# Kernel optimization log

Measured on AMD Instinct MI355X. Metric: run time of the kernel, lower is better.

## Reference

```python
import jax, jax.numpy as jnp
import numpy as np

INPUT_DIM = 1024
HIDDEN_DIM = 2048
NUM_EMB = 4096
EMB_DIM = 256
N = 65536


def setup_inputs() -> dict:
    key = jax.random.key(0)
    ks = jax.random.split(key, 10)
    s = lambda fan_in: 1.0 / np.sqrt(fan_in)
    return {
        "x": jax.random.normal(ks[0], (N, INPUT_DIM), dtype=jnp.float32),
        # encoder: Linear(input_dim, hidden) -> ReLU -> Linear(hidden, emb)
        "W1": jax.random.uniform(ks[1], (INPUT_DIM, HIDDEN_DIM), jnp.float32, -s(INPUT_DIM), s(INPUT_DIM)),
        "b1": jax.random.uniform(ks[2], (HIDDEN_DIM,), jnp.float32, -s(INPUT_DIM), s(INPUT_DIM)),
        "W2": jax.random.uniform(ks[3], (HIDDEN_DIM, EMB_DIM), jnp.float32, -s(HIDDEN_DIM), s(HIDDEN_DIM)),
        "b2": jax.random.uniform(ks[4], (EMB_DIM,), jnp.float32, -s(HIDDEN_DIM), s(HIDDEN_DIM)),
        # codebook (nn.Embedding weight)
        "codebook": jax.random.normal(ks[5], (NUM_EMB, EMB_DIM), dtype=jnp.float32),
        # decoder: Linear(emb, hidden) -> ReLU -> Linear(hidden, input_dim)
        "W3": jax.random.uniform(ks[6], (EMB_DIM, HIDDEN_DIM), jnp.float32, -s(EMB_DIM), s(EMB_DIM)),
        "b3": jax.random.uniform(ks[7], (HIDDEN_DIM,), jnp.float32, -s(EMB_DIM), s(EMB_DIM)),
        "W4": jax.random.uniform(ks[8], (HIDDEN_DIM, INPUT_DIM), jnp.float32, -s(HIDDEN_DIM), s(HIDDEN_DIM)),
        "b4": jax.random.uniform(ks[9], (INPUT_DIM,), jnp.float32, -s(HIDDEN_DIM), s(HIDDEN_DIM)),
    }


def reference(x, W1, b1, W2, b2, codebook, W3, b3, W4, b4):
    # encoder
    h = jax.nn.relu(x @ W1 + b1)
    encoded = h @ W2 + b2                      # [N, E]
    # cdist (squared form; argmin is identical to Euclidean argmin)
    enc_sq = jnp.sum(encoded * encoded, axis=-1, keepdims=True)   # [N, 1]
    cb_sq = jnp.sum(codebook * codebook, axis=-1)                 # [K]
    d2 = enc_sq - 2.0 * (encoded @ codebook.T) + cb_sq            # [N, K]
    indices = jnp.argmin(d2, axis=-1)                             # [N]
    quantized = codebook[indices]                                 # [N, E]
    # decoder
    h2 = jax.nn.relu(quantized @ W3 + b3)
    decoded = h2 @ W4 + b4
    return (quantized, decoded)
```

## Files before the change

### kernel.cpp

```cpp
#include <hip/hip_runtime.h>

#define N_ROWS 65536
#define IN_DIM 1024
#define HID    2048
#define EMB    256
#define NCODE  4096

typedef __attribute__((ext_vector_type(8))) short bf16x8;
typedef __attribute__((ext_vector_type(4))) float f32x4;

__device__ __forceinline__ unsigned short f2bf(float v) {
    unsigned u = __float_as_uint(v);
    u += 0x7FFFu + ((u >> 16) & 1u);
    return (unsigned short)(u >> 16);
}
__device__ __forceinline__ float bf2f(unsigned short h) {
    return __uint_as_float(((unsigned)h) << 16);
}
__device__ __forceinline__ void gload16(const unsigned short* g, unsigned short* l) {
    __builtin_amdgcn_global_load_lds(
        (const __attribute__((address_space(1))) unsigned int*)g,
        (__attribute__((address_space(3))) unsigned int*)l, 16, 0, 0);
}

template<int SPLIT>
__global__ __launch_bounds__(256) void k_conv_w(
    const float* __restrict__ src, unsigned short* __restrict__ dh,
    unsigned short* __restrict__ dl, int NC, int nkt)
{
    const int t = threadIdx.x;
    const int nt = blockIdx.x, kt = blockIdx.y;
    const int kk = t >> 2, j4 = (t & 3) << 2;
    const int k0 = kt << 6, n0 = nt << 4;
    float4 v = *(const float4*)(src + (size_t)(k0 + kk) * NC + n0 + j4);
    size_t tb = ((size_t)nt * nkt + kt) * 1024 + ((kk >> 3) * 128) + (kk & 7);
    float vv[4] = {v.x, v.y, v.z, v.w};
    #pragma unroll
    for (int j = 0; j < 4; ++j) {
        unsigned short h = f2bf(vv[j]);
        dh[tb + (size_t)(j4 + j) * 8] = h;
        if (SPLIT) dl[tb + (size_t)(j4 + j) * 8] = f2bf(vv[j] - bf2f(h));
    }
}

__global__ __launch_bounds__(256) void k_conv_a(
    const float* __restrict__ src, unsigned short* __restrict__ dst, int Kw, int nkt)
{
    const int t = threadIdx.x;
    const int mt = blockIdx.x, kt = blockIdx.y;
    const int rr = t >> 4, k4 = (t & 15) << 2;
    float4 v = *(const float4*)(src + (size_t)(mt * 16 + rr) * Kw + kt * 64 + k4);
    size_t addr = ((size_t)mt * nkt + kt) * 1024 + (k4 >> 3) * 128 + rr * 8 + (k4 & 7);
    ushort4 h = { f2bf(v.x), f2bf(v.y), f2bf(v.z), f2bf(v.w) };
    *(ushort4*)&dst[addr] = h;
}

__global__ __launch_bounds__(256) void k_conv_cb(
    const float* __restrict__ cb, unsigned short* __restrict__ ch,
    unsigned short* __restrict__ cl_, float* __restrict__ halfsq)
{
    const int t = threadIdx.x;
    const int ct = blockIdx.x;
    const int cl = t >> 4, f = t & 15;
    const int code = (ct << 4) + cl;
    float ssq = 0.f;
    #pragma unroll
    for (int it = 0; it < 4; ++it) {
        const int k4 = (f << 2) + (it << 6);
        float4 v = *(const float4*)(cb + (size_t)code * EMB + k4);
        ssq += v.x * v.x + v.y * v.y + v.z * v.z + v.w * v.w;
        size_t tb = ((size_t)(ct * 4 + (k4 >> 6))) * 1024 + ((k4 >> 3) & 7) * 128 + cl * 8 + (k4 & 7);
        ushort4 h = { f2bf(v.x), f2bf(v.y), f2bf(v.z), f2bf(v.w) };
        *(ushort4*)&ch[tb] = h;
        ushort4 lo = { f2bf(v.x - bf2f(h.x)), f2bf(v.y - bf2f(h.y)),
                       f2bf(v.z - bf2f(h.z)), f2bf(v.w - bf2f(h.w)) };
        *(ushort4*)&cl_[tb] = lo;
    }
    #pragma unroll
    for (int off = 1; off <= 8; off <<= 1) ssq += __shfl_xor(ssq, off);
    if (f == 0) halfsq[code] = 0.5f * ssq;
}

template<int SPLIT, int AFMT, int OUTT>
__global__ __launch_bounds__(512, 1) void k_layer2(
    const float* __restrict__ A, const unsigned short* __restrict__ At,
    const unsigned short* __restrict__ Atl, int a_nkt,
    int lda, int K,
    const unsigned short* __restrict__ Bh, const unsigned short* __restrict__ Bl,
    int b_nkt, const float* __restrict__ bias, int biasoff,
    float* __restrict__ out, unsigned short* __restrict__ outt,
    unsigned short* __restrict__ outt2,
    int outw, int relu, int init, int ny_log2)
{
    constexpr int BUFSZ = SPLIT ? 32768 : 24576;
    constexpr int AL = 8192;
    constexpr int BH = SPLIT ? 16384 : 8192;
    __shared__ __align__(16) unsigned short s_mem[2 * BUFSZ];

    const int t = threadIdx.x;
    const int id = blockIdx.x;
    const int m_low = id & 7, rest = id >> 3;
    const int nb = rest & ((1 << ny_log2) - 1);
    const int m0 = (((rest >> ny_log2) << 3) | m_low) * 128;
    const int nb0 = nb * 256;
    const int lane = t & 63, wv = t >> 6;
    const int wm = wv >> 2, wn = wv & 3;
    const int g = lane >> 4, rr = lane & 15;
    const int nt = K >> 6;

    f32x4 acc[4][4];
    #pragma unroll
    for (int mi = 0; mi < 4; ++mi)
        #pragma unroll
        for (int ni = 0; ni < 4; ++ni) acc[mi][ni] = (f32x4){0.f, 0.f, 0.f, 0.f};

    #define STAGE_DMA(buf, ktile)                                                      \
        {                                                                              \
            unsigned short* base_ = &s_mem[(buf) * BUFSZ];                             \
            _Pragma("unroll")                                                          \
            for (int jj = 0; jj < 2; ++jj) {                                           \
                const int j_ = wv * 2 + jj;                                            \
                const size_t gt_ = ((size_t)(nb0 / 16 + j_) * b_nkt + (ktile)) * 1024; \
                _Pragma("unroll")                                                      \
                for (int hf = 0; hf < 2; ++hf)                                         \
                    gload16(Bh + gt_ + hf * 512 + lane * 8,                            \
                            base_ + BH + j_ * 1024 + hf * 512);                        \
            }                                                                          \
            if (AFMT >= 1) {                                                           \
                const size_t ga_ = ((size_t)(m0 / 16 + wv) * a_nkt + (ktile)) * 1024;  \
                _Pragma("unroll")                                                      \
                for (int hf = 0; hf < 2; ++hf)                                         \
                    gload16(At + ga_ + hf * 512 + lane * 8,                            \
                            base_ + wv * 1024 + hf * 512);                             \
                if (AFMT == 2) {                                                       \
                    _Pragma("unroll")                                                  \
                    for (int hf = 0; hf < 2; ++hf)                                     \
                        gload16(Atl + ga_ + hf * 512 + lane * 8,                       \
                                base_ + AL + wv * 1024 + hf * 512);                    \
                }                                                                      \
            }                                                                          \
        }

    #define A_LOAD(ktile, pv)                                                          \
        {                                                                              \
            _Pragma("unroll")                                                          \
            for (int it = 0; it < 4; ++it) {                                           \
                int f_ = t + (it << 9);                                                \
                int r_ = f_ >> 4, k4_ = (f_ & 15) << 2;                                \
                pv[it] = *(const float4*)(A + (size_t)(m0 + r_) * lda + (ktile) * 64 + k4_); \
            }                                                                          \
        }

    #define A_WRITE(buf, pv)                                                           \
        {                                                                              \
            unsigned short* base_ = &s_mem[(buf) * BUFSZ];                             \
            _Pragma("unroll")                                                          \
            for (int it = 0; it < 4; ++it) {                                           \
                int f_ = t + (it << 9);                                                \
                int r_ = f_ >> 4, k4_ = (f_ & 15) << 2;                                \
                int mt_ = r_ >> 4, rl_ = r_ & 15, kb_ = k4_ >> 3, e_ = k4_ & 7;        \
                int addr_ = mt_ * 1024 + kb_ * 128 + ((rl_ ^ kb_) << 3) + e_;          \
                float4 v_ = pv[it];                                                    \
                ushort4 hi_, lo_;                                                      \
                hi_.x = f2bf(v_.x); hi_.y = f2bf(v_.y); hi_.z = f2bf(v_.z); hi_.w = f2bf(v_.w); \
                *(ushort4*)&base_[addr_] = hi_;                                        \
                if (SPLIT) {                                                           \
                    lo_.x = f2bf(v_.x - bf2f(hi_.x)); lo_.y = f2bf(v_.y - bf2f(hi_.y)); \
                    lo_.z = f2bf(v_.z - bf2f(hi_.z)); lo_.w = f2bf(v_.w - bf2f(hi_.w)); \
                    *(ushort4*)&base_[AL + addr_] = lo_;                               \
                }                                                                      \
            }                                                                          \
        }

    #define COMPUTE(buf, ktile)                                                        \
        {                                                                              \
            const unsigned short* base_ = &s_mem[(buf) * BUFSZ];                       \
            __builtin_amdgcn_s_setprio(1);                                             \
            _Pragma("unroll")                                                          \
            for (int s = 0; s < 2; ++s) {                                              \
                const int kb = (s << 2) + g;                                           \
                bf16x8 a_h[4], a_l[4], b_h[4], b_l[4];                                 \
                _Pragma("unroll")                                                      \
                for (int i = 0; i < 4; ++i) {                                          \
                    int arow = (AFMT == 0) ? (((rr ^ kb) & 15) << 3) : (rr << 3);      \
                    int aaddr = (wm * 4 + i) * 1024 + kb * 128 + arow;                 \
                    a_h[i] = *(const bf16x8*)&base_[aaddr];                            \
                    if (SPLIT) a_l[i] = *(const bf16x8*)&base_[AL + aaddr];            \
                    int baddr = (wn * 4 + i) * 1024 + kb * 128 + (rr << 3);            \
                    b_h[i] = *(const bf16x8*)&base_[BH + baddr];                       \
                    if (SPLIT)                                                         \
                        b_l[i] = *(const bf16x8*)(Bl +                                 \
                            ((size_t)(nb0 / 16 + wn * 4 + i) * b_nkt + (ktile)) * 1024 \
                            + kb * 128 + (rr << 3));                                   \
                }                                                                      \
                _Pragma("unroll")                                                      \
                for (int mi = 0; mi < 4; ++mi)                                         \
                    _Pragma("unroll")                                                  \
                    for (int ni = 0; ni < 4; ++ni) {                                   \
                        acc[mi][ni] = __builtin_amdgcn_mfma_f32_16x16x32_bf16(a_h[mi], b_h[ni], acc[mi][ni], 0, 0, 0); \
                        if (SPLIT) {                                                   \
                            acc[mi][ni] = __builtin_amdgcn_mfma_f32_16x16x32_bf16(a_l[mi], b_h[ni], acc[mi][ni], 0, 0, 0); \
                            acc[mi][ni] = __builtin_amdgcn_mfma_f32_16x16x32_bf16(a_h[mi], b_l[ni], acc[mi][ni], 0, 0, 0); \
                        }                                                              \
                    }                                                                  \
            }                                                                          \
            __builtin_amdgcn_s_setprio(0);                                             \
        }

    float4 pv[4];
    STAGE_DMA(0, 0)
    if (AFMT == 0) {
        A_LOAD(0, pv)
        A_WRITE(0, pv)
    }
    asm volatile("s_waitcnt vmcnt(0) lgkmcnt(0)" ::: "memory");
    __builtin_amdgcn_s_barrier();
    __builtin_amdgcn_sched_barrier(0);

    int cur = 0;
    for (int kt = 0; kt < nt; ++kt) {
        if (kt + 1 < nt) {
            STAGE_DMA(cur ^ 1, kt + 1)
            if (AFMT == 0) A_LOAD(kt + 1, pv)
        }
        COMPUTE(cur, kt)
        if (AFMT == 0) { if (kt + 1 < nt) A_WRITE(cur ^ 1, pv) }
        asm volatile("s_waitcnt vmcnt(0) lgkmcnt(0)" ::: "memory");
        __builtin_amdgcn_s_barrier();
        __builtin_amdgcn_sched_barrier(0);
        cur ^= 1;
    }
    #undef STAGE_DMA
    #undef A_LOAD
    #undef A_WRITE
    #undef COMPUTE

    if (OUTT == 0) {
        float* sf = (float*)s_mem;
        for (int rm = 0; rm < 2; ++rm) {
            if (wm == rm) {
                #pragma unroll
                for (int mi = 0; mi < 4; ++mi)
                    #pragma unroll
                    for (int ni = 0; ni < 4; ++ni)
                        #pragma unroll
                        for (int rg = 0; rg < 4; ++rg)
                            sf[(mi * 16 + g * 4 + rg) * 256 + wn * 64 + ni * 16 + rr] = acc[mi][ni][rg];
            }
            __syncthreads();
            #pragma unroll
            for (int it = 0; it < 8; ++it) {
                int f = t + (it << 9);
                int r = f >> 6, c4 = (f & 63) << 2;
                float4 v = *(const float4*)&sf[r * 256 + c4];
                int gr = m0 + rm * 64 + r, gc = nb0 + c4;
                float* op = out + (size_t)gr * outw + gc;
                if (init) {
                    v.x += bias[biasoff + gc + 0]; v.y += bias[biasoff + gc + 1];
                    v.z += bias[biasoff + gc + 2]; v.w += bias[biasoff + gc + 3];
                } else {
                    float4 o = *(const float4*)op;
                    v.x += o.x; v.y += o.y; v.z += o.z; v.w += o.w;
                }
                if (relu) {
                    v.x = fmaxf(v.x, 0.f); v.y = fmaxf(v.y, 0.f);
                    v.z = fmaxf(v.z, 0.f); v.w = fmaxf(v.w, 0.f);
                }
                *(float4*)op = v;
            }
            __syncthreads();
        }
    } else {
        const int npass = (OUTT == 2) ? 2 : 1;
        for (int pass = 0; pass < npass; ++pass) {
            #pragma unroll
            for (int mi = 0; mi < 4; ++mi)
                #pragma unroll
                for (int ni = 0; ni < 4; ++ni) {
                    const int c = wn * 64 + ni * 16 + rr;
                    float bb = bias[biasoff + nb0 + c];
                    #pragma unroll
                    for (int rg = 0; rg < 4; ++rg) {
                        float v = acc[mi][ni][rg] + bb;
                        if (relu) v = fmaxf(v, 0.f);
                        unsigned short hi = f2bf(v);
                        unsigned short w = (pass == 0) ? hi : f2bf(v - bf2f(hi));
                        int addr = ((wm * 4 + mi) * 4 + wn) * 1024
                                 + (ni * 2 + (rr >> 3)) * 128 + (g * 4 + rg) * 8 + (rr & 7);
                        s_mem[addr] = w;
                    }
                }
            __syncthreads();
            unsigned short* dst = (pass == 0) ? outt : outt2;
            #pragma unroll
            for (int it = 0; it < 8; ++it) {
                int f = t + (it << 9);
                int tl = f >> 7, w8 = f & 127;
                size_t gaddr = ((size_t)(m0 / 16 + (tl >> 2)) * outw + nb0 / 64 + (tl & 3)) * 1024;
                *(float4*)(dst + gaddr + w8 * 8) = *(const float4*)&s_mem[tl * 1024 + w8 * 8];
            }
            __syncthreads();
        }
    }
}

__global__ __launch_bounds__(512, 2) void k_dist(
    float* encq, const unsigned short* __restrict__ ch,
    const unsigned short* __restrict__ cl,
    const float* __restrict__ hsq, const float* __restrict__ cb)
{
    __shared__ __align__(16) unsigned short s_cb[2][16384];
    __shared__ int s_c1[256], s_c2[256];

    const int t = threadIdx.x;
    const int lane = t & 63, wv = t >> 6;
    const int g = lane >> 4, rr = lane & 15;
    const int r0 = blockIdx.x * 256;

    bf16x8 eh[2][8], el[2][8];
    #pragma unroll
    for (int rg = 0; rg < 2; ++rg) {
        const float* ep = encq + (size_t)(r0 + wv * 32 + rg * 16 + rr) * EMB + g * 8;
        #pragma unroll
        for (int s = 0; s < 8; ++s) {
            float4 v0 = *(const float4*)(ep + s * 32);
            float4 v1 = *(const float4*)(ep + s * 32 + 4);
            float vv[8] = {v0.x, v0.y, v0.z, v0.w, v1.x, v1.y, v1.z, v1.w};
            bf16x8 a, b;
            #pragma unroll
            for (int j = 0; j < 8; ++j) {
                unsigned short h = f2bf(vv[j]);
                a[j] = (short)h;
                b[j] = (short)f2bf(vv[j] - bf2f(h));
            }
            eh[rg][s] = a; el[rg][s] = b;
        }
    }
    float b1v[2][4], b2v[2][4]; int i1v[2][4], i2v[2][4];
    #pragma unroll
    for (int rg = 0; rg < 2; ++rg)
        #pragma unroll
        for (int r2 = 0; r2 < 4; ++r2) {
            b1v[rg][r2] = -1e30f; b2v[rg][r2] = -1e30f;
            i1v[rg][r2] = 0; i2v[rg][r2] = 0;
        }

    #define STAGE(buf, c)                                                              \
        {                                                                              \
            const unsigned short* gh_ = ch + (size_t)(c) * 8192 + wv * 1024;           \
            const unsigned short* gl_ = cl + (size_t)(c) * 8192 + wv * 1024;           \
            _Pragma("unroll")                                                          \
            for (int i_ = 0; i_ < 2; ++i_) {                                           \
                gload16(gh_ + i_ * 512 + lane * 8, &s_cb[buf][wv * 1024 + i_ * 512]);  \
                gload16(gl_ + i_ * 512 + lane * 8, &s_cb[buf][8192 + wv * 1024 + i_ * 512]); \
            }                                                                          \
        }

    #define COMPUTE(cur, c, hv_)                                                       \
        {                                                                              \
            f32x4 ahh[2][2], ahl[2][2], alh[2][2];                                     \
            _Pragma("unroll")                                                          \
            for (int rg = 0; rg < 2; ++rg)                                             \
                _Pragma("unroll")                                                      \
                for (int ci = 0; ci < 2; ++ci) {                                       \
                    ahh[rg][ci] = (f32x4){0.f, 0.f, 0.f, 0.f};                         \
                    ahl[rg][ci] = (f32x4){0.f, 0.f, 0.f, 0.f};                         \
                    alh[rg][ci] = (f32x4){0.f, 0.f, 0.f, 0.f};                         \
                }                                                                      \
            __builtin_amdgcn_s_setprio(1);                                             \
            _Pragma("unroll")                                                          \
            for (int s = 0; s < 8; ++s) {                                              \
                const int ktile = s >> 1, kb = ((s & 1) << 2) + g;                     \
                _Pragma("unroll")                                                      \
                for (int ci = 0; ci < 2; ++ci) {                                       \
                    const int off = (ci * 4 + ktile) * 1024 + kb * 128 + rr * 8;       \
                    bf16x8 bh = *(const bf16x8*)&s_cb[cur][off];                       \
                    bf16x8 bl = *(const bf16x8*)&s_cb[cur][8192 + off];                \
                    _Pragma("unroll")                                                  \
                    for (int rg = 0; rg < 2; ++rg) {                                   \
                        ahh[rg][ci] = __builtin_amdgcn_mfma_f32_16x16x32_bf16(eh[rg][s], bh, ahh[rg][ci], 0, 0, 0); \
                        ahl[rg][ci] = __builtin_amdgcn_mfma_f32_16x16x32_bf16(eh[rg][s], bl, ahl[rg][ci], 0, 0, 0); \
                        alh[rg][ci] = __builtin_amdgcn_mfma_f32_16x16x32_bf16(el[rg][s], bh, alh[rg][ci], 0, 0, 0); \
                    }                                                                  \
                }                                                                      \
            }                                                                          \
            __builtin_amdgcn_s_setprio(0);                                             \
            _Pragma("unroll")                                                          \
            for (int rg = 0; rg < 2; ++rg)                                             \
                _Pragma("unroll")                                                      \
                for (int ci = 0; ci < 2; ++ci) {                                       \
                    f32x4 av = ahh[rg][ci] + ahl[rg][ci] + alh[rg][ci];                \
                    const int code = ((c) << 5) + (ci << 4) + rr;                      \
                    const float hs = __shfl(hv_, ci * 16 + rr);                        \
                    _Pragma("unroll")                                                  \
                    for (int r2 = 0; r2 < 4; ++r2) {                                   \
                        float v = av[r2] - hs;                                         \
                        bool bt1 = (v > b1v[rg][r2]) || (v == b1v[rg][r2] && code < i1v[rg][r2]); \
                        bool bt2 = (v > b2v[rg][r2]) || (v == b2v[rg][r2] && code < i2v[rg][r2]); \
                        if (bt1) { b2v[rg][r2] = b1v[rg][r2]; i2v[rg][r2] = i1v[rg][r2]; \
                                   b1v[rg][r2] = v; i1v[rg][r2] = code; }              \
                        else if (bt2) { b2v[rg][r2] = v; i2v[rg][r2] = code; }         \
                    }                                                                  \
                }                                                                      \
        }

    STAGE(0, 0)
    int cur = 0;
    for (int c = 0; c < 127; ++c) {
        STAGE(cur ^ 1, c + 1)
        float hv_ = hsq[(c << 5) + (lane & 31)];
        asm volatile("s_waitcnt vmcnt(5)" ::: "memory");
        __builtin_amdgcn_s_barrier();
        __builtin_amdgcn_sched_barrier(0);
        COMPUTE(cur, c, hv_)
        asm volatile("" ::: "memory");
        __builtin_amdgcn_s_barrier();
        cur ^= 1;
    }
    {
        float hv_ = hsq[(127 << 5) + (lane & 31)];
        asm volatile("s_waitcnt vmcnt(0)" ::: "memory");
        __builtin_amdgcn_s_barrier();
        __builtin_amdgcn_sched_barrier(0);
        COMPUTE(cur, 127, hv_)
    }
    #undef STAGE
    #undef COMPUTE

    #pragma unroll
    for (int off = 1; off <= 8; off <<= 1) {
        #pragma unroll
        for (int rg = 0; rg < 2; ++rg)
            #pragma unroll
            for (int r2 = 0; r2 < 4; ++r2) {
                float ob1 = __shfl_xor(b1v[rg][r2], off), ob2 = __shfl_xor(b2v[rg][r2], off);
                int oi1 = __shfl_xor(i1v[rg][r2], off), oi2 = __shfl_xor(i2v[rg][r2], off);
                bool ofirst = (ob1 > b1v[rg][r2]) || (ob1 == b1v[rg][r2] && oi1 < i1v[rg][r2]);
                if (ofirst) {
                    bool mysec = (b1v[rg][r2] > ob2) || (b1v[rg][r2] == ob2 && i1v[rg][r2] < oi2);
                    b2v[rg][r2] = mysec ? b1v[rg][r2] : ob2; i2v[rg][r2] = mysec ? i1v[rg][r2] : oi2;
                    b1v[rg][r2] = ob1; i1v[rg][r2] = oi1;
                } else {
                    bool osec = (ob1 > b2v[rg][r2]) || (ob1 == b2v[rg][r2] && oi1 < i2v[rg][r2]);
                    b2v[rg][r2] = osec ? ob1 : b2v[rg][r2]; i2v[rg][r2] = osec ? oi1 : i2v[rg][r2];
                }
            }
    }
    if (rr == 0) {
        #pragma unroll
        for (int rg = 0; rg < 2; ++rg)
            #pragma unroll
            for (int r2 = 0; r2 < 4; ++r2) {
                int rl = wv * 32 + rg * 16 + g * 4 + r2;
                s_c1[rl] = i1v[rg][r2]; s_c2[rl] = i2v[rg][r2];
            }
    }
    __syncthreads();

    for (int rloc = 0; rloc < 32; ++rloc) {
        const int row = wv * 32 + rloc;
        const int c1 = s_c1[row], c2 = s_c2[row];
        float4 ev = *(const float4*)(encq + (size_t)(r0 + row) * EMB + lane * 4);
        float4 v1 = *(const float4*)(cb + (size_t)c1 * EMB + lane * 4);
        float4 v2 = *(const float4*)(cb + (size_t)c2 * EMB + lane * 4);
        float d1 = ev.x * v1.x + ev.y * v1.y + ev.z * v1.z + ev.w * v1.w;
        float d2 = ev.x * v2.x + ev.y * v2.y + ev.z * v2.z + ev.w * v2.w;
        #pragma unroll
        for (int off = 1; off <= 32; off <<= 1) {
            d1 += __shfl_xor(d1, off);
            d2 += __shfl_xor(d2, off);
        }
        if (lane == 0) {
            float s1 = d1 - hsq[c1], s2 = d2 - hsq[c2];
            bool keep1 = (s1 > s2) || (s1 == s2 && c1 < c2);
            s_c1[row] = keep1 ? c1 : c2;
        }
    }
    __syncthreads();
    #pragma unroll
    for (int it = 0; it < 32; ++it) {
        int f = t + (it << 9);
        int row = f >> 6, c4 = (f & 63) << 2;
        int bi = s_c1[row];
        *(float4*)(encq + (size_t)(r0 + row) * EMB + c4) =
            *(const float4*)(cb + (size_t)bi * EMB + c4);
    }
}

__global__ __launch_bounds__(256) void k_dec_fb(
    const float* __restrict__ qz,
    const float* __restrict__ W3, const float* __restrict__ b3,
    const float* __restrict__ W4, const float* __restrict__ b4,
    float* __restrict__ outd) {
    __shared__ float s_q[8][EMB];
    __shared__ float s_h2[8][HID];
    const int t = threadIdx.x;
    const int row0 = blockIdx.x * 8;
    #pragma unroll
    for (int r = 0; r < 8; ++r) s_q[r][t] = qz[(size_t)(row0 + r) * EMB + t];
    __syncthreads();
    for (int gg = 0; gg < 8; ++gg) {
        const int j = (gg << 8) + t;
        float acc[8];
        #pragma unroll
        for (int r = 0; r < 8; ++r) acc[r] = 0.f;
        const float* wp = W3 + j;
        for (int e = 0; e < EMB; e += 4) {
            const float w0 = wp[(size_t)(e + 0) * HID];
            const float w1v = wp[(size_t)(e + 1) * HID];
            const float w2v = wp[(size_t)(e + 2) * HID];
            const float w3v = wp[(size_t)(e + 3) * HID];
            #pragma unroll
            for (int r = 0; r < 8; ++r) {
                const float4 qv = *reinterpret_cast<const float4*>(&s_q[r][e]);
                acc[r] = fmaf(qv.x, w0, acc[r]);
                acc[r] = fmaf(qv.y, w1v, acc[r]);
                acc[r] = fmaf(qv.z, w2v, acc[r]);
                acc[r] = fmaf(qv.w, w3v, acc[r]);
            }
        }
        const float bb = b3[j];
        #pragma unroll
        for (int r = 0; r < 8; ++r) s_h2[r][j] = fmaxf(acc[r] + bb, 0.f);
    }
    __syncthreads();
    float acc4[8][4];
    #pragma unroll
    for (int r = 0; r < 8; ++r)
        #pragma unroll
        for (int ci = 0; ci < 4; ++ci) acc4[r][ci] = 0.f;
    const float* w4p = W4 + t;
    for (int k = 0; k < HID; k += 4) {
        float wv[4][4];
        #pragma unroll
        for (int ki = 0; ki < 4; ++ki)
            #pragma unroll
            for (int ci = 0; ci < 4; ++ci)
                wv[ki][ci] = w4p[(size_t)(k + ki) * IN_DIM + (ci << 8)];
        #pragma unroll
        for (int r = 0; r < 8; ++r) {
            const float4 hv = *reinterpret_cast<const float4*>(&s_h2[r][k]);
            #pragma unroll
            for (int ci = 0; ci < 4; ++ci) {
                acc4[r][ci] = fmaf(hv.x, wv[0][ci], acc4[r][ci]);
                acc4[r][ci] = fmaf(hv.y, wv[1][ci], acc4[r][ci]);
                acc4[r][ci] = fmaf(hv.z, wv[2][ci], acc4[r][ci]);
                acc4[r][ci] = fmaf(hv.w, wv[3][ci], acc4[r][ci]);
            }
        }
    }
    #pragma unroll
    for (int ci = 0; ci < 4; ++ci) {
        const float bb = b4[(ci << 8) + t];
        #pragma unroll
        for (int r = 0; r < 8; ++r)
            outd[(size_t)(row0 + r) * IN_DIM + (ci << 8) + t] = acc4[r][ci] + bb;
    }
}

extern "C" void kernel_launch(void* const* d_in, const int* in_sizes, int n_in,
                              void* d_out, int out_size, void* d_ws, size_t ws_size,
                              hipStream_t stream) {
    const float* x  = (const float*)d_in[0];
    const float* W1 = (const float*)d_in[1];
    const float* b1 = (const float*)d_in[2];
    const float* W2 = (const float*)d_in[3];
    const float* b2 = (const float*)d_in[4];
    const float* cb = (const float*)d_in[5];
    const float* W3 = (const float*)d_in[6];
    const float* b3 = (const float*)d_in[7];
    const float* W4 = (const float*)d_in[8];
    const float* b4 = (const float*)d_in[9];

    float* outq = (float*)d_out;
    float* outd = outq + (size_t)N_ROWS * EMB;

    unsigned short* ou = (unsigned short*)outd;
    unsigned short* W1Th = ou;
    unsigned short* W1Tl = ou + 2097152;
    unsigned short* W2Th = ou + 4194304;
    unsigned short* W2Tl = ou + 4718592;
    unsigned short* cbh  = ou + 5242880;
    unsigned short* cbl  = ou + 6291456;
    float* halfsq = outd + 3670016;
    unsigned short* h_hi = (unsigned short*)(outd + 4194304);
    unsigned short* h_lo = h_hi + 33554432;
    unsigned short* qt = (unsigned short*)(outd + 58720256);
    float* enc = outq;

    const bool fastdec = ws_size >= (size_t)72351744;
    unsigned short* W3Th = (unsigned short*)d_ws;
    unsigned short* W4Th = W3Th + 524288;
    unsigned short* h2t  = (unsigned short*)((char*)d_ws + 5242880);

    k_conv_w<1><<<dim3(128, 16), 256, 0, stream>>>(W1, W1Th, W1Tl, HID, 16);
    k_conv_w<1><<<dim3(16, 32), 256, 0, stream>>>(W2, W2Th, W2Tl, EMB, 32);
    k_conv_cb<<<256, 256, 0, stream>>>(cb, cbh, cbl, halfsq);
    if (fastdec) {
        k_conv_w<0><<<dim3(128, 4), 256, 0, stream>>>(W3, W3Th, nullptr, HID, 4);
        k_conv_w<0><<<dim3(64, 32), 256, 0, stream>>>(W4, W4Th, nullptr, IN_DIM, 32);
    }
    for (int q = 0; q < 4; ++q) {
        k_layer2<1, 0, 2><<<1024, 512, 0, stream>>>(
            x, nullptr, nullptr, 0, IN_DIM, IN_DIM,
            W1Th + (size_t)q * 524288, W1Tl + (size_t)q * 524288, 16,
            b1, q * 512, nullptr, h_hi, h_lo, 8, 1, 0, 1);
        k_layer2<1, 2, 0><<<512, 512, 0, stream>>>(
            nullptr, h_hi, h_lo, 8, 0, 512,
            W2Th + (size_t)q * 8192, W2Tl + (size_t)q * 8192, 32,
            b2, 0, enc, nullptr, nullptr, EMB, 0, q == 0, 0);
    }
    k_dist<<<256, 512, 0, stream>>>(enc, cbh, cbl, halfsq, cb);
    if (fastdec) {
        k_conv_a<<<dim3(4096, 4), 256, 0, stream>>>(outq, qt, EMB, 4);
        for (int s = 0; s < 4; ++s) {
            const size_t roff = (size_t)s * 16384;
            k_layer2<0, 1, 1><<<1024, 512, 0, stream>>>(
                nullptr, qt + (size_t)s * 4194304, nullptr, 4, 0, EMB,
                W3Th, nullptr, 4,
                b3, 0, nullptr, h2t, nullptr, 32, 1, 0, 3);
            k_layer2<0, 1, 0><<<512, 512, 0, stream>>>(
                nullptr, h2t, nullptr, 32, 0, HID,
                W4Th, nullptr, 32,
                b4, 0, outd + roff * IN_DIM, nullptr, nullptr, IN_DIM, 0, 1, 2);
        }
    } else {
        k_dec_fb<<<N_ROWS / 8, 256, 0, stream>>>(outq, W3, b3, W4, b4, outd);
    }
}
```

Baseline: 2.374 ms.

## Pre-convert x to split bf16 tiles and chunk encoder by row blocks

Adds a kernel that converts each quarter of x into pre-tiled hi/lo bf16 buffers. The encoder is then restructured from four hidden-dim column chunks into four row chunks, so each chunk computes the full hidden width and writes its slice of the embedding directly instead of accumulating partial sums across passes. This is meant to remove the repeated fp32 reads and conversion of x in every layer-1 pass and the read-modify-write accumulation into enc. In exchange it adds extra conversion launches and workspace traffic, and it only takes effect when the workspace is large enough.

```diff
diff --git a/kernel.cpp b/kernel.cpp
--- a/kernel.cpp
+++ b/kernel.cpp
@@ -53,6 +53,22 @@
     size_t addr = ((size_t)mt * nkt + kt) * 1024 + (k4 >> 3) * 128 + rr * 8 + (k4 & 7);
     ushort4 h = { f2bf(v.x), f2bf(v.y), f2bf(v.z), f2bf(v.w) };
     *(ushort4*)&dst[addr] = h;
+}
+
+__global__ __launch_bounds__(256) void k_conv_a2(
+    const float* __restrict__ src, unsigned short* __restrict__ dh,
+    unsigned short* __restrict__ dl, int Kw, int nkt)
+{
+    const int t = threadIdx.x;
+    const int mt = blockIdx.x, kt = blockIdx.y;
+    const int rr = t >> 4, k4 = (t & 15) << 2;
+    float4 v = *(const float4*)(src + (size_t)(mt * 16 + rr) * Kw + kt * 64 + k4);
+    size_t addr = ((size_t)mt * nkt + kt) * 1024 + (k4 >> 3) * 128 + rr * 8 + (k4 & 7);
+    ushort4 h = { f2bf(v.x), f2bf(v.y), f2bf(v.z), f2bf(v.w) };
+    ushort4 lo = { f2bf(v.x - bf2f(h.x)), f2bf(v.y - bf2f(h.y)),
+                   f2bf(v.z - bf2f(h.z)), f2bf(v.w - bf2f(h.w)) };
+    *(ushort4*)&dh[addr] = h;
+    *(ushort4*)&dl[addr] = lo;
 }
 
 __global__ __launch_bounds__(256) void k_conv_cb(
@@ -592,6 +608,8 @@
     unsigned short* W3Th = (unsigned short*)d_ws;
     unsigned short* W4Th = W3Th + 524288;
     unsigned short* h2t  = (unsigned short*)((char*)d_ws + 5242880);
+    unsigned short* xt_hi = h2t;
+    unsigned short* xt_lo = h2t + 16777216;
 
     k_conv_w<1><<<dim3(128, 16), 256, 0, stream>>>(W1, W1Th, W1Tl, HID, 16);
     k_conv_w<1><<<dim3(16, 32), 256, 0, stream>>>(W2, W2Th, W2Tl, EMB, 32);
@@ -600,15 +618,30 @@
         k_conv_w<0><<<dim3(128, 4), 256, 0, stream>>>(W3, W3Th, nullptr, HID, 4);
         k_conv_w<0><<<dim3(64, 32), 256, 0, stream>>>(W4, W4Th, nullptr, IN_DIM, 32);
     }
-    for (int q = 0; q < 4; ++q) {
-        k_layer2<1, 0, 2><<<1024, 512, 0, stream>>>(
-            x, nullptr, nullptr, 0, IN_DIM, IN_DIM,
-            W1Th + (size_t)q * 524288, W1Tl + (size_t)q * 524288, 16,
-            b1, q * 512, nullptr, h_hi, h_lo, 8, 1, 0, 1);
-        k_layer2<1, 2, 0><<<512, 512, 0, stream>>>(
-            nullptr, h_hi, h_lo, 8, 0, 512,
-            W2Th + (size_t)q * 8192, W2Tl + (size_t)q * 8192, 32,
-            b2, 0, enc, nullptr, nullptr, EMB, 0, q == 0, 0);
+    if (fastdec) {
+        for (int s = 0; s < 4; ++s) {
+            k_conv_a2<<<dim3(1024, 16), 256, 0, stream>>>(
+                x + (size_t)s * 16777216, xt_hi, xt_lo, IN_DIM, 16);
+            k_layer2<1, 2, 2><<<1024, 512, 0, stream>>>(
+                nullptr, xt_hi, xt_lo, 16, 0, IN_DIM,
+                W1Th, W1Tl, 16, b1, 0,
+                nullptr, h_hi, h_lo, 32, 1, 0, 3);
+            k_layer2<1, 2, 0><<<128, 512, 0, stream>>>(
+                nullptr, h_hi, h_lo, 32, 0, HID,
+                W2Th, W2Tl, 32, b2, 0,
+                enc + (size_t)s * 4194304, nullptr, nullptr, EMB, 0, 1, 0);
+        }
+    } else {
+        for (int q = 0; q < 4; ++q) {
+            k_layer2<1, 0, 2><<<1024, 512, 0, stream>>>(
+                x, nullptr, nullptr, 0, IN_DIM, IN_DIM,
+                W1Th + (size_t)q * 524288, W1Tl + (size_t)q * 524288, 16,
+                b1, q * 512, nullptr, h_hi, h_lo, 8, 1, 0, 1);
+            k_layer2<1, 2, 0><<<512, 512, 0, stream>>>(
+                nullptr, h_hi, h_lo, 8, 0, 512,
+                W2Th + (size_t)q * 8192, W2Tl + (size_t)q * 8192, 32,
+                b2, 0, enc, nullptr, nullptr, EMB, 0, q == 0, 0);
+        }
     }
     k_dist<<<256, 512, 0, stream>>>(enc, cbh, cbl, halfsq, cb);
     if (fastdec) {
```

Measured after the change: 2.359 ms. Within noise of the previous version (-0.6%).
